# Kernel tuning notes

Measured on AMD Instinct MI355X. Metric: run time of the kernel, lower is better.

Reference implementation:

```python
import jax, jax.numpy as jnp
import numpy as np

MODES = 2
LC = 4
N = 6000
KNN = 10
NODES = 64
CH = MODES ** 2
M = N * 2 * (KNN + 1)  # total candidate couplings


def setup_inputs() -> dict:
    key = jax.random.key(0)
    ks = jax.random.split(key, 6)
    return {
        "CK_inputs": jax.random.normal(ks[0], (N, 2 * (KNN + 1), 3), dtype=jnp.float32),
        "W_in": jax.random.normal(ks[1], (3, NODES), dtype=jnp.float32) * 0.1,
        "b_in": jnp.zeros((NODES,), dtype=jnp.float32),
        "W_hid": jax.random.normal(ks[2], (LC - 1, NODES, NODES), dtype=jnp.float32) * 0.1,
        "b_hid": jnp.zeros((LC - 1, NODES), dtype=jnp.float32),
        "W_out": jax.random.normal(ks[3], (NODES, CH), dtype=jnp.float32) * 0.1,
        "b_out": jnp.zeros((CH,), dtype=jnp.float32),
        "coo": jax.random.randint(ks[4], (2, M), 0, N, dtype=jnp.int32),
    }


def _mlp(x, W_in, b_in, W_hid, b_hid, W_out, b_out):
    # MLP: 3 -> 64, (LC-1) hidden 64->64 layers, 64 -> CH; ReLU activations.
    h = jax.nn.relu(x @ W_in + b_in)
    for i in range(W_hid.shape[0]):  # small fixed layer count
        h = jax.nn.relu(h @ W_hid[i] + b_hid[i])
    return h @ W_out + b_out  # [M, CH]


def reference(CK_inputs, W_in, b_in, W_hid, b_hid, W_out, b_out, coo):
    C_stripped = _mlp(CK_inputs.reshape(-1, 3), W_in, b_in, W_hid, b_hid, W_out, b_out)  # [M, CH]
    D = MODES * N
    # Original: for channel ch = mi*MODES+mj, scatter C_stripped[:, ch] at indices coo*MODES+mj
    # (mj added to BOTH row and col, replicating the source exactly). Indices are
    # independent of mi, so sum over mi first, then one scatter-add per mj.
    vals = C_stripped.reshape(-1, MODES, MODES).sum(axis=1)  # [M, MODES]; axis1=mi, axis2=mj
    dense = jnp.zeros((D, D), dtype=CK_inputs.dtype)
    for mj in range(MODES):
        idx = coo * MODES + mj  # [2, M]
        dense = dense.at[idx[0], idx[1]].add(vals[:, mj])
    return dense
```

## Files before the change

kernel.cpp:

```cpp
#include <hip/hip_runtime.h>
#include <stdint.h>

#define NN    6000
#define KNNC  10
#define MM    (NN * 2 * (KNNC + 1))
#define DD    (2 * NN)
#define LCH   3
#define BLK   256

#define NV        ((long long)DD * DD / 4)
#define FILLGRID  2048
#define MLPGRID   ((MM + BLK - 1) / BLK)


__global__ __launch_bounds__(BLK) void zero_fill(float* __restrict__ out) {
    const long long t0 = (long long)blockIdx.x * BLK + threadIdx.x;
    const long long stride = (long long)FILLGRID * BLK;
    float4 z = make_float4(0.f, 0.f, 0.f, 0.f);
    float4* outv = (float4*)out;
    for (long long i = t0; i < NV; i += stride) outv[i] = z;
}

__global__ __launch_bounds__(BLK) void mlp(
    const float* __restrict__ CK,
    const float* __restrict__ Win,
    const float* __restrict__ bin,
    const float* __restrict__ Whid,
    const float* __restrict__ bhid,
    const float* __restrict__ Wout,
    const float* __restrict__ bout,
    float* __restrict__ vals)
{
    __shared__ float sH[64 * BLK];

    const int tid = threadIdx.x;
    const int m0  = blockIdx.x * BLK + tid;
    const int m   = m0 < MM ? m0 : MM - 1;

    const float x0 = CK[m * 3 + 0];
    const float x1 = CK[m * 3 + 1];
    const float x2 = CK[m * 3 + 2];

    float* __restrict__ hcol = sH + tid;

#pragma unroll
    for (int j = 0; j < 64; j++) {
        float a = bin[j];
        a = fmaf(x0, Win[j],       a);
        a = fmaf(x1, Win[64 + j],  a);
        a = fmaf(x2, Win[128 + j], a);
        hcol[j * BLK] = fmaxf(a, 0.0f);
    }

#pragma unroll 1
    for (int l = 0; l < LCH; l++) {
        const float4* __restrict__ W4 = (const float4*)(Whid + (l << 12));
        const float*  __restrict__ bh = bhid + (l << 6);
        float g[64];
#pragma unroll
        for (int j = 0; j < 64; j++) g[j] = bh[j];
#pragma unroll 8
        for (int k = 0; k < 64; k++) {
            const float hk = hcol[k * BLK];
            const float4* __restrict__ Wk = W4 + (k << 4);
#pragma unroll
            for (int j4 = 0; j4 < 16; j4++) {
                float4 w = Wk[j4];
                g[j4 * 4 + 0] = fmaf(w.x, hk, g[j4 * 4 + 0]);
                g[j4 * 4 + 1] = fmaf(w.y, hk, g[j4 * 4 + 1]);
                g[j4 * 4 + 2] = fmaf(w.z, hk, g[j4 * 4 + 2]);
                g[j4 * 4 + 3] = fmaf(w.w, hk, g[j4 * 4 + 3]);
            }
        }
#pragma unroll
        for (int j = 0; j < 64; j++) hcol[j * BLK] = fmaxf(g[j], 0.0f);
    }

    float v0 = bout[0] + bout[2];
    float v1 = bout[1] + bout[3];
#pragma unroll 8
    for (int k = 0; k < 64; k++) {
        float4 wo = *((const float4*)Wout + k);
        const float hk = hcol[k * BLK];
        v0 = fmaf(hk, wo.x + wo.z, v0);
        v1 = fmaf(hk, wo.y + wo.w, v1);
    }
    if (m0 < MM) *(float2*)(vals + 2 * m0) = make_float2(v0, v1);
}

__global__ __launch_bounds__(BLK) void scatter_add(
    const float* __restrict__ vals,
    const int* __restrict__ coo,
    float* __restrict__ out)
{
    const int t = blockIdx.x * BLK + threadIdx.x;
    if (t >= MM) return;
    const int r2 = coo[t] * 2;
    const int c2 = coo[MM + t] * 2;
    const float2 v = *(const float2*)(vals + 2 * t);
    const long long f0 = (long long)r2 * DD + c2;
    unsafeAtomicAdd(out + f0, v.x);
    unsafeAtomicAdd(out + f0 + DD + 1, v.y);
}

extern "C" void kernel_launch(void* const* d_in, const int* in_sizes, int n_in,
                              void* d_out, int out_size, void* d_ws, size_t ws_size,
                              hipStream_t stream) {
    const float* CK   = (const float*)d_in[0];
    const float* Win  = (const float*)d_in[1];
    const float* bin  = (const float*)d_in[2];
    const float* Whid = (const float*)d_in[3];
    const float* bhid = (const float*)d_in[4];
    const float* Wout = (const float*)d_in[5];
    const float* bout = (const float*)d_in[6];
    const int* coo    = (const int*)d_in[7];
    float* out        = (float*)d_out;
    float* vals       = (float*)d_ws;

    mlp<<<MLPGRID, BLK, 0, stream>>>(CK, Win, bin, Whid, bhid, Wout, bout, vals);
    zero_fill<<<FILLGRID, BLK, 0, stream>>>(out);
    scatter_add<<<MLPGRID, BLK, 0, stream>>>(vals, coo, out);
}
```

Baseline: 744.0 us.

## Register-block MLP rows and stage hidden weights in shared memory

The MLP kernel is reorganised so each thread computes 16 output features for 4 rows, instead of all 64 features for a single row. Each block stages the 64x64 hidden-layer weight matrix in shared memory, and block-wide barriers separate layer updates of the shared activation buffer. This raises arithmetic reuse per activation load and moves weight reads from global/scalar loads to LDS. The cost is extra barriers and LDS traffic. The end-to-end time is likely dominated by the large dense zero-fill, which this change does not touch.

```diff
diff --git a/kernel.cpp b/kernel.cpp
--- a/kernel.cpp
+++ b/kernel.cpp
@@ -10,8 +10,10 @@
 
 #define NV        ((long long)DD * DD / 4)
 #define FILLGRID  2048
-#define MLPGRID   ((MM + BLK - 1) / BLK)
-
+#define RB        256
+#define RPL       4
+#define MLPGRID   ((MM + RB - 1) / RB)
+#define SCGRID    ((MM + BLK - 1) / BLK)
 
 __global__ __launch_bounds__(BLK) void zero_fill(float* __restrict__ out) {
     const long long t0 = (long long)blockIdx.x * BLK + threadIdx.x;
@@ -21,7 +23,7 @@
     for (long long i = t0; i < NV; i += stride) outv[i] = z;
 }
 
-__global__ __launch_bounds__(BLK) void mlp(
+__global__ __launch_bounds__(BLK, 2) void mlp(
     const float* __restrict__ CK,
     const float* __restrict__ Win,
     const float* __restrict__ bin,
@@ -31,61 +33,116 @@
     const float* __restrict__ bout,
     float* __restrict__ vals)
 {
-    __shared__ float sH[64 * BLK];
+    __shared__ float sW[64 * 64];
+    __shared__ float sH[64 * RB];
 
-    const int tid = threadIdx.x;
-    const int m0  = blockIdx.x * BLK + tid;
-    const int m   = m0 < MM ? m0 : MM - 1;
+    const int tid   = threadIdx.x;
+    const int wave  = tid >> 6;
+    const int lane  = tid & 63;
+    const int jo    = wave << 4;
+    const int rbase = blockIdx.x * RB;
 
-    const float x0 = CK[m * 3 + 0];
-    const float x1 = CK[m * 3 + 1];
-    const float x2 = CK[m * 3 + 2];
-
-    float* __restrict__ hcol = sH + tid;
+    float x0[RPL], x1[RPL], x2[RPL];
+#pragma unroll
+    for (int r = 0; r < RPL; r++) {
+        int m = rbase + r * 64 + lane;
+        m = m < MM ? m : MM - 1;
+        x0[r] = CK[m * 3 + 0];
+        x1[r] = CK[m * 3 + 1];
+        x2[r] = CK[m * 3 + 2];
+    }
 
 #pragma unroll
-    for (int j = 0; j < 64; j++) {
-        float a = bin[j];
-        a = fmaf(x0, Win[j],       a);
-        a = fmaf(x1, Win[64 + j],  a);
-        a = fmaf(x2, Win[128 + j], a);
-        hcol[j * BLK] = fmaxf(a, 0.0f);
+    for (int jj = 0; jj < 16; jj++) {
+        const int j = jo + jj;
+        const float w0 = Win[j], w1 = Win[64 + j], w2 = Win[128 + j];
+        const float bj = bin[j];
+#pragma unroll
+        for (int r = 0; r < RPL; r++) {
+            float a = fmaf(x2[r], w2, fmaf(x1[r], w1, fmaf(x0[r], w0, bj)));
+            sH[j * RB + r * 64 + lane] = fmaxf(a, 0.f);
+        }
     }
+    __syncthreads();
 
 #pragma unroll 1
     for (int l = 0; l < LCH; l++) {
-        const float4* __restrict__ W4 = (const float4*)(Whid + (l << 12));
-        const float*  __restrict__ bh = bhid + (l << 6);
-        float g[64];
+        {
+            const float4* __restrict__ Wg = (const float4*)(Whid + (l << 12));
+            float4* __restrict__ sW4 = (float4*)sW;
 #pragma unroll
-        for (int j = 0; j < 64; j++) g[j] = bh[j];
-#pragma unroll 8
+            for (int i = 0; i < 4; i++) sW4[i * 256 + tid] = Wg[i * 256 + tid];
+        }
+        __syncthreads();
+
+        float g[RPL][16];
+#pragma unroll
+        for (int jj = 0; jj < 16; jj++) {
+            const float bj = bhid[(l << 6) + jo + jj];
+#pragma unroll
+            for (int r = 0; r < RPL; r++) g[r][jj] = bj;
+        }
+
+#pragma unroll 4
         for (int k = 0; k < 64; k++) {
-            const float hk = hcol[k * BLK];
-            const float4* __restrict__ Wk = W4 + (k << 4);
+            const float4 wa = *(const float4*)(sW + (k << 6) + jo);
+            const float4 wb = *(const float4*)(sW + (k << 6) + jo + 4);
+            const float4 wc = *(const float4*)(sW + (k << 6) + jo + 8);
+            const float4 wd = *(const float4*)(sW + (k << 6) + jo + 12);
+            float hk[RPL];
 #pragma unroll
-            for (int j4 = 0; j4 < 16; j4++) {
-                float4 w = Wk[j4];
-                g[j4 * 4 + 0] = fmaf(w.x, hk, g[j4 * 4 + 0]);
-                g[j4 * 4 + 1] = fmaf(w.y, hk, g[j4 * 4 + 1]);
-                g[j4 * 4 + 2] = fmaf(w.z, hk, g[j4 * 4 + 2]);
-                g[j4 * 4 + 3] = fmaf(w.w, hk, g[j4 * 4 + 3]);
+            for (int r = 0; r < RPL; r++) hk[r] = sH[k * RB + r * 64 + lane];
+#pragma unroll
+            for (int r = 0; r < RPL; r++) {
+                g[r][0]  = fmaf(wa.x, hk[r], g[r][0]);
+                g[r][1]  = fmaf(wa.y, hk[r], g[r][1]);
+                g[r][2]  = fmaf(wa.z, hk[r], g[r][2]);
+                g[r][3]  = fmaf(wa.w, hk[r], g[r][3]);
+                g[r][4]  = fmaf(wb.x, hk[r], g[r][4]);
+                g[r][5]  = fmaf(wb.y, hk[r], g[r][5]);
+                g[r][6]  = fmaf(wb.z, hk[r], g[r][6]);
+                g[r][7]  = fmaf(wb.w, hk[r], g[r][7]);
+                g[r][8]  = fmaf(wc.x, hk[r], g[r][8]);
+                g[r][9]  = fmaf(wc.y, hk[r], g[r][9]);
+                g[r][10] = fmaf(wc.z, hk[r], g[r][10]);
+                g[r][11] = fmaf(wc.w, hk[r], g[r][11]);
+                g[r][12] = fmaf(wd.x, hk[r], g[r][12]);
+                g[r][13] = fmaf(wd.y, hk[r], g[r][13]);
+                g[r][14] = fmaf(wd.z, hk[r], g[r][14]);
+                g[r][15] = fmaf(wd.w, hk[r], g[r][15]);
             }
         }
+        __syncthreads();
+
 #pragma unroll
-        for (int j = 0; j < 64; j++) hcol[j * BLK] = fmaxf(g[j], 0.0f);
+        for (int jj = 0; jj < 16; jj++) {
+#pragma unroll
+            for (int r = 0; r < RPL; r++)
+                sH[(jo + jj) * RB + r * 64 + lane] = fmaxf(g[r][jj], 0.f);
+        }
+        __syncthreads();
     }
 
-    float v0 = bout[0] + bout[2];
-    float v1 = bout[1] + bout[3];
+    float v0[RPL], v1[RPL];
+    const float b02 = bout[0] + bout[2], b13 = bout[1] + bout[3];
+#pragma unroll
+    for (int r = 0; r < RPL; r++) { v0[r] = b02; v1[r] = b13; }
 #pragma unroll 8
     for (int k = 0; k < 64; k++) {
-        float4 wo = *((const float4*)Wout + k);
-        const float hk = hcol[k * BLK];
-        v0 = fmaf(hk, wo.x + wo.z, v0);
-        v1 = fmaf(hk, wo.y + wo.w, v1);
+        const float4 wo = ((const float4*)Wout)[k];
+        const float wxz = wo.x + wo.z, wyw = wo.y + wo.w;
+#pragma unroll
+        for (int r = 0; r < RPL; r++) {
+            const float hk = sH[k * RB + r * 64 + lane];
+            v0[r] = fmaf(hk, wxz, v0[r]);
+            v1[r] = fmaf(hk, wyw, v1[r]);
+        }
     }
-    if (m0 < MM) *(float2*)(vals + 2 * m0) = make_float2(v0, v1);
+#pragma unroll
+    for (int r = 0; r < RPL; r++) {
+        const int m = rbase + r * 64 + lane;
+        if (m < MM) *(float2*)(vals + 2 * m) = make_float2(v0[r], v1[r]);
+    }
 }
 
 __global__ __launch_bounds__(BLK) void scatter_add(
@@ -119,5 +176,5 @@
 
     mlp<<<MLPGRID, BLK, 0, stream>>>(CK, Win, bin, Whid, bhid, Wout, bout, vals);
     zero_fill<<<FILLGRID, BLK, 0, stream>>>(out);
-    scatter_add<<<MLPGRID, BLK, 0, stream>>>(vals, coo, out);
+    scatter_add<<<SCGRID, BLK, 0, stream>>>(vals, coo, out);
 }
```

Result: faster. 699.3 us (-6.0%).
